# Kernel tuning notes

Hardware: AMD Instinct MI355X
Metric: run time of the kernel (lower is better)

The kernel has to match this reference:

```python
import jax, jax.numpy as jnp
import numpy as np

DIM = 1024
HEADS = 8
DIM_HEAD = 64
HIDDEN = HEADS * DIM_HEAD  # 512
SCALE = DIM_HEAD ** -0.5
BATCH = 16384
EPS = 1e-12  # F.normalize eps


def setup_inputs() -> dict:
    key = jax.random.key(0)
    k0, k1, k2 = jax.random.split(key, 3)
    x = jax.random.normal(k0, (BATCH, DIM), dtype=jnp.float32)
    w_qkv = jax.random.normal(k1, (3 * HIDDEN, DIM), dtype=jnp.float32) * 0.02
    w_out = jax.random.normal(k2, (DIM, HIDDEN), dtype=jnp.float32) * 0.02
    b_out = jnp.zeros((DIM,), dtype=jnp.float32)
    g = jnp.ones((1, DIM), dtype=jnp.float32)
    return {"x": x, "w_qkv": w_qkv, "w_out": w_out, "b_out": b_out, "g": g}


def reference(x, w_qkv, w_out, b_out, g):
    b = x.shape[0]
    # Conv1d(kernel=1, no bias) on n=1 sequence == matmul with (3*hidden, dim) weight
    qkv = x @ w_qkv.T  # (b, 3*hidden)
    q, k, v = jnp.split(qkv, 3, axis=1)  # each (b, hidden)
    # rearrange 'b (h c) n -> b h c n' with n=1 -> (b, h, c)
    q = q.reshape(b, HEADS, DIM_HEAD)
    k = k.reshape(b, HEADS, DIM_HEAD)
    v = v.reshape(b, HEADS, DIM_HEAD)
    # q.softmax(dim=-2) is over the c axis
    q = jax.nn.softmax(q, axis=-1) * SCALE
    # k.softmax(dim=-1) is over the n axis of size 1 -> all ones (kept faithful)
    k = jax.nn.softmax(k[..., None], axis=-1)[..., 0]
    # context = einsum('bhdn,bhen->bhde', k, v); out = einsum('bhde,bhdn->bhen', context, q)
    # with n=1 this collapses to out_e = (sum_d k_d q_d) * v_e; fused to avoid (b,h,d,e)
    s = jnp.einsum('bhd,bhd->bh', k, q)  # (b, h)
    out = s[..., None] * v  # (b, h, e)
    out = out.reshape(b, HIDDEN)  # 'b h c n -> b (h c) n', squeeze(-1)
    # Linear(hidden, dim)
    out = out @ w_out.T + b_out  # (b, dim)
    # RMSNorm_MLP: F.normalize(x, dim=1) * g * sqrt(dim)
    norm = jnp.linalg.norm(out, axis=1, keepdims=True)
    out = out / jnp.maximum(norm, EPS) * g * jnp.sqrt(jnp.float32(DIM))
    return out
```

## Files before the change

kernel.cpp:

```cpp
#include <hip/hip_runtime.h>
#include <hip/hip_bf16.h>


typedef __attribute__((ext_vector_type(8))) short bf16x8;
typedef __attribute__((ext_vector_type(4))) float f32x4;

struct alignas(16) bfvec8 { __hip_bfloat16 h[8]; };

__device__ __forceinline__ bfvec8 pack8(float4 a, float4 b) {
    bfvec8 o;
    o.h[0] = __float2bfloat16(a.x); o.h[1] = __float2bfloat16(a.y);
    o.h[2] = __float2bfloat16(a.z); o.h[3] = __float2bfloat16(a.w);
    o.h[4] = __float2bfloat16(b.x); o.h[5] = __float2bfloat16(b.y);
    o.h[6] = __float2bfloat16(b.z); o.h[7] = __float2bfloat16(b.w);
    return o;
}

__global__ __launch_bounds__(256)
void prep(const float* __restrict__ Wo, const float* __restrict__ Wv,
          __hip_bfloat16* __restrict__ Weff,
          const float* __restrict__ X, __hip_bfloat16* __restrict__ Xbf) {
    __shared__ __align__(16) __hip_bfloat16 As[64 * 32];
    __shared__ __align__(16) __hip_bfloat16 Bs[64 * 32];
    __shared__ __align__(16) float Bf[32 * 65];

    const int tid = threadIdx.x;

    if (blockIdx.x >= 256) {
        const size_t nv = (size_t)16384 * 1024 / 8;
        const size_t stride = (size_t)2048 * 256;
        for (size_t i = (size_t)(blockIdx.x - 256) * 256 + tid; i < nv; i += stride) {
            const float4 a = *(const float4*)(X + i * 8);
            const float4 b = *(const float4*)(X + i * 8 + 4);
            *(bfvec8*)(Xbf + i * 8) = pack8(a, b);
        }
        return;
    }

    const int lane = tid & 63;
    const int wave = tid >> 6;
    const int wm   = wave >> 1;
    const int wn   = wave & 1;
    const int quad = lane >> 4;
    const int tr   = lane & 15;
    const int m0   = (blockIdx.x >> 4) * 64;
    const int n0   = (blockIdx.x & 15) * 64;

    f32x4 acc[2][2];
#pragma unroll
    for (int i = 0; i < 2; ++i)
#pragma unroll
        for (int j = 0; j < 2; ++j)
            acc[i][j] = (f32x4){0.f, 0.f, 0.f, 0.f};

    for (int kt = 0; kt < 512; kt += 32) {
        {
            int r = tid >> 2, c = tid & 3;
            int s = (r >> 1) & 3;
            int kg = (c ^ s) << 3;
            const float* sp = Wo + (size_t)(m0 + r) * 512 + kt + kg;
            float4 a = *(const float4*)sp, b = *(const float4*)(sp + 4);
            *(bfvec8*)(As + r * 32 + (c << 3)) = pack8(a, b);
        }
        {
            int kr = tid >> 3, c8 = (tid & 7) << 3;
            const float* sp = Wv + (size_t)(kt + kr) * 1024 + n0 + c8;
            float4 a = *(const float4*)sp, b = *(const float4*)(sp + 4);
            *(float4*)(Bf + kr * 65 + c8)     = a;
            *(float4*)(Bf + kr * 65 + c8 + 4) = b;
        }
        __syncthreads();
        {
            int n = tid >> 2, cc = tid & 3, k8 = cc << 3;
            float4 a, b;
            a.x = Bf[(k8 + 0) * 65 + n]; a.y = Bf[(k8 + 1) * 65 + n];
            a.z = Bf[(k8 + 2) * 65 + n]; a.w = Bf[(k8 + 3) * 65 + n];
            b.x = Bf[(k8 + 4) * 65 + n]; b.y = Bf[(k8 + 5) * 65 + n];
            b.z = Bf[(k8 + 6) * 65 + n]; b.w = Bf[(k8 + 7) * 65 + n];
            int cs = cc ^ ((n >> 1) & 3);
            *(bfvec8*)(Bs + n * 32 + cs * 8) = pack8(a, b);
        }
        __syncthreads();

        bf16x8 af[2], bfr[2];
#pragma unroll
        for (int mi = 0; mi < 2; ++mi) {
            int r = wm * 32 + mi * 16 + tr;
            int c = quad ^ ((r >> 1) & 3);
            af[mi] = *(const bf16x8*)(As + r * 32 + c * 8);
        }
#pragma unroll
        for (int ni = 0; ni < 2; ++ni) {
            int r = wn * 32 + ni * 16 + tr;
            int c = quad ^ ((r >> 1) & 3);
            bfr[ni] = *(const bf16x8*)(Bs + r * 32 + c * 8);
        }
#pragma unroll
        for (int mi = 0; mi < 2; ++mi)
#pragma unroll
            for (int ni = 0; ni < 2; ++ni)
                acc[mi][ni] = __builtin_amdgcn_mfma_f32_16x16x32_bf16(
                    af[mi], bfr[ni], acc[mi][ni], 0, 0, 0);
        __syncthreads();
    }

#pragma unroll
    for (int mi = 0; mi < 2; ++mi)
#pragma unroll
        for (int ni = 0; ni < 2; ++ni) {
            const int col = n0 + wn * 32 + ni * 16 + tr;
#pragma unroll
            for (int r = 0; r < 4; ++r) {
                const int row = m0 + wm * 32 + mi * 16 + quad * 4 + r;
                Weff[(size_t)row * 1024 + col] =
                    __float2bfloat16(acc[mi][ni][r] * 0.125f);
            }
        }
}


#define GLL(gp, lp) __builtin_amdgcn_global_load_lds( \
    (const __attribute__((address_space(1))) void*)(gp), \
    (__attribute__((address_space(3))) void*)(lp), 16, 0, 0)

#define STAGE_A(BUF, H, U) do { \
    GLL(Xbf + Ab0 + (size_t)(H) * 131072 + (size_t)(U) * 64, \
        sm + (BUF) * 32768 + (H) * 8192 + ldsA);             \
    GLL(Xbf + Ab1 + (size_t)(H) * 131072 + (size_t)(U) * 64, \
        sm + (BUF) * 32768 + (H) * 8192 + 4096 + ldsA);      \
} while (0)

#define STAGE_B(BUF, H, U) do { \
    GLL(Bt + Bb0 + (size_t)(H) * 131072 + (size_t)(U) * 64,  \
        sm + (BUF) * 32768 + 16384 + (H) * 8192 + ldsA);     \
    GLL(Bt + Bb1 + (size_t)(H) * 131072 + (size_t)(U) * 64,  \
        sm + (BUF) * 32768 + 16384 + (H) * 8192 + 4096 + ldsA); \
} while (0)

__global__ __launch_bounds__(512, 2)
void main_gemm(const __hip_bfloat16* __restrict__ Xbf,
               const __hip_bfloat16* __restrict__ Bt,
               const float* __restrict__ bias,
               __hip_bfloat16* __restrict__ Y) {
    __shared__ __align__(16) __hip_bfloat16 sm[2 * 32768];

    const int tid  = threadIdx.x;
    const int lane = tid & 63;
    const int wc   = tid >> 6;
    const int quad = lane >> 4;
    const int tr   = lane & 15;
    const int rlow = tr & 7;

    const int xcd  = blockIdx.x & 7;
    const int orig = xcd * 32 + (blockIdx.x >> 3);
    const int m0   = (orig >> 2) * 256;
    const int n0   = (orig & 3) * 256;

    const int r0 = tid >> 3,            c0 = tid & 7;
    const int r1 = (tid + 512) >> 3,    c1 = tid & 7;
    const size_t Ab0 = (size_t)(m0 + r0) * 1024 + ((c0 ^ (r0 & 7)) << 3);
    const size_t Ab1 = (size_t)(m0 + r1) * 1024 + ((c1 ^ (r1 & 7)) << 3);
    const size_t Bb0 = (size_t)(n0 + r0) * 1024 + ((c0 ^ (r0 & 7)) << 3);
    const size_t Bb1 = (size_t)(n0 + r1) * 1024 + ((c1 ^ (r1 & 7)) << 3);
    const int ldsA = tid * 8;

    int ac[2];
#pragma unroll
    for (int ko = 0; ko < 2; ++ko) ac[ko] = ((ko * 4 + quad) ^ rlow) * 8;
    const int rdA = tr * 64;
    const int rdB = wc * 2048 + tr * 64;

    f32x4 acc[16][2];
#pragma unroll
    for (int f = 0; f < 16; ++f)
#pragma unroll
        for (int ni = 0; ni < 2; ++ni)
            acc[f][ni] = (f32x4){0.f, 0.f, 0.f, 0.f};

    STAGE_B(0, 0, 0); STAGE_B(0, 1, 0); STAGE_A(0, 0, 0); STAGE_A(0, 1, 0);
    STAGE_B(1, 0, 1); STAGE_B(1, 1, 1); STAGE_A(1, 0, 1);
    asm volatile("s_waitcnt vmcnt(6)" ::: "memory");
    __builtin_amdgcn_s_barrier();

    bf16x8 bfr[2][2];

    for (int it = 0; it < 8; ++it) {
#pragma unroll
        for (int rb = 0; rb < 2; ++rb) {
            const int u = it * 2 + rb;
#pragma unroll
            for (int p = 0; p < 4; ++p) {
                bf16x8 af[4][2];
#pragma unroll
                for (int mi = 0; mi < 4; ++mi)
#pragma unroll
                    for (int ko = 0; ko < 2; ++ko)
                        af[mi][ko] = *(const bf16x8*)(
                            sm + rb * 32768 + p * 4096 + mi * 1024 + rdA + ac[ko]);
                if (p == 0) {
#pragma unroll
                    for (int ni = 0; ni < 2; ++ni)
#pragma unroll
                        for (int ko = 0; ko < 2; ++ko)
                            bfr[ni][ko] = *(const bf16x8*)(
                                sm + rb * 32768 + 16384 + rdB + ni * 1024 + ac[ko]);
                }

                if (p == 0)      { if (u + 1 < 16) STAGE_A(rb ^ 1, 1, u + 1); }
                else if (p == 1) { if (u + 2 < 16) STAGE_B(rb, 0, u + 2); }
                else if (p == 2) { if (u + 2 < 16) STAGE_B(rb, 1, u + 2); }
                else             { if (u + 2 < 16) STAGE_A(rb, 0, u + 2); }

                if (p == 0) asm volatile("s_waitcnt lgkmcnt(8)" ::: "memory");
                __builtin_amdgcn_s_barrier();
                asm volatile("s_waitcnt lgkmcnt(0)" ::: "memory");
                __builtin_amdgcn_sched_barrier(0);

                __builtin_amdgcn_s_setprio(1);
#pragma unroll
                for (int mi = 0; mi < 4; ++mi)
#pragma unroll
                    for (int ni = 0; ni < 2; ++ni)
#pragma unroll
                        for (int ko = 0; ko < 2; ++ko)
                            acc[p * 4 + mi][ni] = __builtin_amdgcn_mfma_f32_16x16x32_bf16(
                                af[mi][ko], bfr[ni][ko], acc[p * 4 + mi][ni], 0, 0, 0);
                __builtin_amdgcn_s_setprio(0);

                if (p == 3) {
                    if (u <= 13)      asm volatile("s_waitcnt vmcnt(6)" ::: "memory");
                    else if (u == 14) asm volatile("s_waitcnt vmcnt(0)" ::: "memory");
                    if (u < 15) __builtin_amdgcn_s_barrier();
                } else {
                    __builtin_amdgcn_s_barrier();
                }
            }
        }
    }

    float bv[2]; int col[2];
#pragma unroll
    for (int ni = 0; ni < 2; ++ni) {
        col[ni] = n0 + wc * 32 + ni * 16 + tr;
        bv[ni]  = bias[col[ni]];
    }
#pragma unroll
    for (int f = 0; f < 16; ++f)
#pragma unroll
        for (int ni = 0; ni < 2; ++ni)
#pragma unroll
            for (int rr = 0; rr < 4; ++rr) {
                const int row = m0 + f * 16 + quad * 4 + rr;
                Y[(size_t)row * 1024 + col[ni]] =
                    __float2bfloat16(acc[f][ni][rr] + bv[ni]);
            }
}

__global__ __launch_bounds__(256)
void rmsnorm2(const __hip_bfloat16* __restrict__ y, const float* __restrict__ g,
              float* __restrict__ out) {
    const int wave = threadIdx.x >> 6;
    const int sub  = wave >> 1;
    const int t    = threadIdx.x & 127;
    const int row  = blockIdx.x * 2 + sub;
    const size_t base = (size_t)row * 1024 + t * 8;

    union { uint4 u; ushort s[8]; } U;
    U.u = *(const uint4*)(y + base);
    float v[8];
#pragma unroll
    for (int j = 0; j < 8; ++j)
        v[j] = __bfloat162float(*(const __hip_bfloat16*)&U.s[j]);

    float ss = 0.f;
#pragma unroll
    for (int j = 0; j < 8; ++j) ss += v[j] * v[j];
#pragma unroll
    for (int off = 32; off > 0; off >>= 1)
        ss += __shfl_down(ss, off, 64);

    __shared__ float wsum[4];
    if ((threadIdx.x & 63) == 0) wsum[wave] = ss;
    __syncthreads();
    const float total = wsum[sub * 2] + wsum[sub * 2 + 1];
    const float sc = 32.0f / fmaxf(sqrtf(total), 1e-12f);

    const float4 g0 = *(const float4*)(g + t * 8);
    const float4 g1 = *(const float4*)(g + t * 8 + 4);
    float4 o0, o1;
    o0.x = v[0] * sc * g0.x; o0.y = v[1] * sc * g0.y;
    o0.z = v[2] * sc * g0.z; o0.w = v[3] * sc * g0.w;
    o1.x = v[4] * sc * g1.x; o1.y = v[5] * sc * g1.y;
    o1.z = v[6] * sc * g1.z; o1.w = v[7] * sc * g1.w;
    *(float4*)(out + base)     = o0;
    *(float4*)(out + base + 4) = o1;
}

extern "C" void kernel_launch(void* const* d_in, const int* in_sizes, int n_in,
                              void* d_out, int out_size, void* d_ws, size_t ws_size,
                              hipStream_t stream) {
    const float* x     = (const float*)d_in[0];
    const float* w_qkv = (const float*)d_in[1];
    const float* w_out = (const float*)d_in[2];
    const float* b_out = (const float*)d_in[3];
    const float* g     = (const float*)d_in[4];

    const int B = 16384, D = 1024, H = 512;
    const float* wv = w_qkv + (size_t)2 * H * D;

    char* ws = (char*)d_ws;
    size_t off = 0;
    __hip_bfloat16* weff_bf = (__hip_bfloat16*)(ws + off); off += (size_t)D * D * 2;
    __hip_bfloat16* y_bf    = (__hip_bfloat16*)(ws + off); off += (size_t)B * D * 2;
    __hip_bfloat16* x_bf    = (__hip_bfloat16*)(ws + off); off += (size_t)B * D * 2;

    prep<<<256 + 2048, 256, 0, stream>>>(w_out, wv, weff_bf, x, x_bf);
    main_gemm<<<256, 512, 0, stream>>>(x_bf, weff_bf, b_out, y_bf);
    rmsnorm2<<<B / 2, 256, 0, stream>>>(y_bf, g, (float*)d_out);
}
```

Measured before the change: 178.4 us.

## Fuse RMSNorm into GEMM epilogue via cooperative grid sync

```diff
diff --git a/kernel.cpp b/kernel.cpp
--- a/kernel.cpp
+++ b/kernel.cpp
@@ -1,5 +1,8 @@
 #include <hip/hip_runtime.h>
 #include <hip/hip_bf16.h>
+#include <hip/hip_cooperative_groups.h>
+
+namespace cg = cooperative_groups;
 
 
 typedef __attribute__((ext_vector_type(8))) short bf16x8;
@@ -138,11 +141,15 @@
 } while (0)
 
 __global__ __launch_bounds__(512, 2)
-void main_gemm(const __hip_bfloat16* __restrict__ Xbf,
-               const __hip_bfloat16* __restrict__ Bt,
-               const float* __restrict__ bias,
-               __hip_bfloat16* __restrict__ Y) {
+void main_fused(const __hip_bfloat16* __restrict__ Xbf,
+                const __hip_bfloat16* __restrict__ Bt,
+                const float* __restrict__ bias,
+                const float* __restrict__ g,
+                float* __restrict__ partial,
+                float* __restrict__ out) {
     __shared__ __align__(16) __hip_bfloat16 sm[2 * 32768];
+    __shared__ float wpart[8][256];
+    __shared__ float scs[256];
 
     const int tid  = threadIdx.x;
     const int lane = tid & 63;
@@ -155,6 +162,7 @@
     const int orig = xcd * 32 + (blockIdx.x >> 3);
     const int m0   = (orig >> 2) * 256;
     const int n0   = (orig & 3) * 256;
+    const int ntl  = orig & 3;
 
     const int r0 = tid >> 3,            c0 = tid & 7;
     const int r1 = (tid + 512) >> 3,    c1 = tid & 7;
@@ -247,53 +255,49 @@
 #pragma unroll
     for (int f = 0; f < 16; ++f)
 #pragma unroll
-        for (int ni = 0; ni < 2; ++ni)
-#pragma unroll
-            for (int rr = 0; rr < 4; ++rr) {
-                const int row = m0 + f * 16 + quad * 4 + rr;
-                Y[(size_t)row * 1024 + col[ni]] =
-                    __float2bfloat16(acc[f][ni][rr] + bv[ni]);
+        for (int rr = 0; rr < 4; ++rr) {
+            float v = 0.f;
+#pragma unroll
+            for (int ni = 0; ni < 2; ++ni) {
+                acc[f][ni][rr] += bv[ni];
+                v += acc[f][ni][rr] * acc[f][ni][rr];
             }
-}
-
-__global__ __launch_bounds__(256)
-void rmsnorm2(const __hip_bfloat16* __restrict__ y, const float* __restrict__ g,
-              float* __restrict__ out) {
-    const int wave = threadIdx.x >> 6;
-    const int sub  = wave >> 1;
-    const int t    = threadIdx.x & 127;
-    const int row  = blockIdx.x * 2 + sub;
-    const size_t base = (size_t)row * 1024 + t * 8;
-
-    union { uint4 u; ushort s[8]; } U;
-    U.u = *(const uint4*)(y + base);
-    float v[8];
-#pragma unroll
-    for (int j = 0; j < 8; ++j)
-        v[j] = __bfloat162float(*(const __hip_bfloat16*)&U.s[j]);
-
-    float ss = 0.f;
-#pragma unroll
-    for (int j = 0; j < 8; ++j) ss += v[j] * v[j];
-#pragma unroll
-    for (int off = 32; off > 0; off >>= 1)
-        ss += __shfl_down(ss, off, 64);
-
-    __shared__ float wsum[4];
-    if ((threadIdx.x & 63) == 0) wsum[wave] = ss;
+#pragma unroll
+            for (int msk = 1; msk < 16; msk <<= 1)
+                v += __shfl_xor(v, msk, 64);
+            if (tr == 0) wpart[wc][f * 16 + quad * 4 + rr] = v;
+        }
     __syncthreads();
-    const float total = wsum[sub * 2] + wsum[sub * 2 + 1];
-    const float sc = 32.0f / fmaxf(sqrtf(total), 1e-12f);
-
-    const float4 g0 = *(const float4*)(g + t * 8);
-    const float4 g1 = *(const float4*)(g + t * 8 + 4);
-    float4 o0, o1;
-    o0.x = v[0] * sc * g0.x; o0.y = v[1] * sc * g0.y;
-    o0.z = v[2] * sc * g0.z; o0.w = v[3] * sc * g0.w;
-    o1.x = v[4] * sc * g1.x; o1.y = v[5] * sc * g1.y;
-    o1.z = v[6] * sc * g1.z; o1.w = v[7] * sc * g1.w;
-    *(float4*)(out + base)     = o0;
-    *(float4*)(out + base + 4) = o1;
+    if (tid < 256) {
+        float s = 0.f;
+#pragma unroll
+        for (int w = 0; w < 8; ++w) s += wpart[w][tid];
+        partial[(size_t)(m0 + tid) * 4 + ntl] = s;
+    }
+
+    cg::this_grid().sync();
+
+    if (tid < 256) {
+        const float* pr = partial + (size_t)(m0 + tid) * 4;
+        const float s = pr[0] + pr[1] + pr[2] + pr[3];
+        scs[tid] = 32.0f / fmaxf(sqrtf(s), 1e-12f);
+    }
+    __syncthreads();
+
+    float gv[2];
+#pragma unroll
+    for (int ni = 0; ni < 2; ++ni) gv[ni] = g[col[ni]];
+#pragma unroll
+    for (int f = 0; f < 16; ++f)
+#pragma unroll
+        for (int rr = 0; rr < 4; ++rr) {
+            const int rowin = f * 16 + quad * 4 + rr;
+            const float sc = scs[rowin];
+#pragma unroll
+            for (int ni = 0; ni < 2; ++ni)
+                out[(size_t)(m0 + rowin) * 1024 + col[ni]] =
+                    acc[f][ni][rr] * sc * gv[ni];
+        }
 }
 
 extern "C" void kernel_launch(void* const* d_in, const int* in_sizes, int n_in,
@@ -311,10 +315,20 @@
     char* ws = (char*)d_ws;
     size_t off = 0;
     __hip_bfloat16* weff_bf = (__hip_bfloat16*)(ws + off); off += (size_t)D * D * 2;
-    __hip_bfloat16* y_bf    = (__hip_bfloat16*)(ws + off); off += (size_t)B * D * 2;
     __hip_bfloat16* x_bf    = (__hip_bfloat16*)(ws + off); off += (size_t)B * D * 2;
+    float*          part    = (float*)(ws + off);          off += (size_t)B * 4 * 4;
 
     prep<<<256 + 2048, 256, 0, stream>>>(w_out, wv, weff_bf, x, x_bf);
-    main_gemm<<<256, 512, 0, stream>>>(x_bf, weff_bf, b_out, y_bf);
-    rmsnorm2<<<B / 2, 256, 0, stream>>>(y_bf, g, (float*)d_out);
+
+    {
+        const __hip_bfloat16* a0 = x_bf;
+        const __hip_bfloat16* a1 = weff_bf;
+        const float* a2 = b_out;
+        const float* a3 = g;
+        float* a4 = part;
+        float* a5 = (float*)d_out;
+        void* args[] = {&a0, &a1, &a2, &a3, &a4, &a5};
+        hipLaunchCooperativeKernel((void*)main_fused, dim3(256), dim3(512),
+                                   args, 0, stream);
+    }
 }
```

Result: slower. 223.0 us (+25.0%).

## Fuse fp32-to-bf16 conversion of X into the main GEMM's A-tile loading

Applied to the files above, without the earlier changes.

```diff
diff --git a/kernel.cpp b/kernel.cpp
--- a/kernel.cpp
+++ b/kernel.cpp
@@ -17,26 +17,13 @@
 }
 
 __global__ __launch_bounds__(256)
-void prep(const float* __restrict__ Wo, const float* __restrict__ Wv,
-          __hip_bfloat16* __restrict__ Weff,
-          const float* __restrict__ X, __hip_bfloat16* __restrict__ Xbf) {
+void weff_only(const float* __restrict__ Wo, const float* __restrict__ Wv,
+               __hip_bfloat16* __restrict__ Weff) {
     __shared__ __align__(16) __hip_bfloat16 As[64 * 32];
     __shared__ __align__(16) __hip_bfloat16 Bs[64 * 32];
     __shared__ __align__(16) float Bf[32 * 65];
 
-    const int tid = threadIdx.x;
-
-    if (blockIdx.x >= 256) {
-        const size_t nv = (size_t)16384 * 1024 / 8;
-        const size_t stride = (size_t)2048 * 256;
-        for (size_t i = (size_t)(blockIdx.x - 256) * 256 + tid; i < nv; i += stride) {
-            const float4 a = *(const float4*)(X + i * 8);
-            const float4 b = *(const float4*)(X + i * 8 + 4);
-            *(bfvec8*)(Xbf + i * 8) = pack8(a, b);
-        }
-        return;
-    }
-
+    const int tid  = threadIdx.x;
     const int lane = tid & 63;
     const int wave = tid >> 6;
     const int wm   = wave >> 1;
@@ -123,22 +110,31 @@
     (const __attribute__((address_space(1))) void*)(gp), \
     (__attribute__((address_space(3))) void*)(lp), 16, 0, 0)
 
-#define STAGE_A(BUF, H, U) do { \
-    GLL(Xbf + Ab0 + (size_t)(H) * 131072 + (size_t)(U) * 64, \
-        sm + (BUF) * 32768 + (H) * 8192 + ldsA);             \
-    GLL(Xbf + Ab1 + (size_t)(H) * 131072 + (size_t)(U) * 64, \
-        sm + (BUF) * 32768 + (H) * 8192 + 4096 + ldsA);      \
-} while (0)
-
 #define STAGE_B(BUF, H, U) do { \
     GLL(Bt + Bb0 + (size_t)(H) * 131072 + (size_t)(U) * 64,  \
-        sm + (BUF) * 32768 + 16384 + (H) * 8192 + ldsA);     \
+        sm + (BUF) * 32768 + 16384 + (H) * 8192 + tid * 8);  \
     GLL(Bt + Bb1 + (size_t)(H) * 131072 + (size_t)(U) * 64,  \
-        sm + (BUF) * 32768 + 16384 + (H) * 8192 + 4096 + ldsA); \
+        sm + (BUF) * 32768 + 16384 + (H) * 8192 + 4096 + tid * 8); \
 } while (0)
 
+#define LOAD_A(U) do { \
+    _Pragma("unroll") \
+    for (int j = 0; j < 4; ++j) { \
+        const float* s_ = Xrow + (size_t)(U) * 64 + aoff[j]; \
+        pa[2*j]   = *(const float4*)s_; \
+        pa[2*j+1] = *(const float4*)(s_ + 4); \
+    } \
+} while (0)
+
+#define WRITE_A(BUF) do { \
+    _Pragma("unroll") \
+    for (int j = 0; j < 4; ++j) \
+        *(bfvec8*)(sm + (BUF) * 32768 + tid * 32 + j * 8) = \
+            pack8(pa[2*j], pa[2*j+1]); \
+} while (0)
+
 __global__ __launch_bounds__(512, 2)
-void main_gemm(const __hip_bfloat16* __restrict__ Xbf,
+void main_gemm(const float* __restrict__ X,
                const __hip_bfloat16* __restrict__ Bt,
                const float* __restrict__ bias,
                __hip_bfloat16* __restrict__ Y) {
@@ -156,13 +152,17 @@
     const int m0   = (orig >> 2) * 256;
     const int n0   = (orig & 3) * 256;
 
-    const int r0 = tid >> 3,            c0 = tid & 7;
-    const int r1 = (tid + 512) >> 3,    c1 = tid & 7;
-    const size_t Ab0 = (size_t)(m0 + r0) * 1024 + ((c0 ^ (r0 & 7)) << 3);
-    const size_t Ab1 = (size_t)(m0 + r1) * 1024 + ((c1 ^ (r1 & 7)) << 3);
+    const int r0 = tid >> 3,         c0 = tid & 7;
+    const int r1 = (tid + 512) >> 3, c1 = tid & 7;
     const size_t Bb0 = (size_t)(n0 + r0) * 1024 + ((c0 ^ (r0 & 7)) << 3);
     const size_t Bb1 = (size_t)(n0 + r1) * 1024 + ((c1 ^ (r1 & 7)) << 3);
-    const int ldsA = tid * 8;
+
+    const int  Ra   = tid >> 1;
+    const float* Xrow = X + (size_t)(m0 + Ra) * 1024;
+    int aoff[4];
+#pragma unroll
+    for (int j = 0; j < 4; ++j)
+        aoff[j] = ((((tid & 1) * 4 + j) ^ (Ra & 7)) << 3);
 
     int ac[2];
 #pragma unroll
@@ -177,9 +177,19 @@
         for (int ni = 0; ni < 2; ++ni)
             acc[f][ni] = (f32x4){0.f, 0.f, 0.f, 0.f};
 
-    STAGE_B(0, 0, 0); STAGE_B(0, 1, 0); STAGE_A(0, 0, 0); STAGE_A(0, 1, 0);
-    STAGE_B(1, 0, 1); STAGE_B(1, 1, 1); STAGE_A(1, 0, 1);
-    asm volatile("s_waitcnt vmcnt(6)" ::: "memory");
+    float4 pa[8];
+
+    LOAD_A(0);
+    __builtin_amdgcn_sched_barrier(0);
+    STAGE_B(0, 0, 0); STAGE_B(0, 1, 0);
+    STAGE_B(1, 0, 1); STAGE_B(1, 1, 1);
+    __builtin_amdgcn_sched_barrier(0);
+    asm volatile("s_waitcnt vmcnt(8)" ::: "memory");
+    WRITE_A(0);
+    __builtin_amdgcn_sched_barrier(0);
+    LOAD_A(1);
+    __builtin_amdgcn_sched_barrier(0);
+    asm volatile("s_waitcnt vmcnt(8) lgkmcnt(0)" ::: "memory");
     __builtin_amdgcn_s_barrier();
 
     bf16x8 bfr[2][2];
@@ -206,10 +216,19 @@
                                 sm + rb * 32768 + 16384 + rdB + ni * 1024 + ac[ko]);
                 }
 
-                if (p == 0)      { if (u + 1 < 16) STAGE_A(rb ^ 1, 1, u + 1); }
-                else if (p == 1) { if (u + 2 < 16) STAGE_B(rb, 0, u + 2); }
-                else if (p == 2) { if (u + 2 < 16) STAGE_B(rb, 1, u + 2); }
-                else             { if (u + 2 < 16) STAGE_A(rb, 0, u + 2); }
+                if (p == 1)      { if (u <= 13) STAGE_B(rb, 0, u + 2); }
+                else if (p == 2) { if (u <= 13) STAGE_B(rb, 1, u + 2); }
+                else if (p == 3) {
+                    if (u <= 14) {
+                        if (u <= 13) asm volatile("s_waitcnt vmcnt(4)" ::: "memory");
+                        else         asm volatile("s_waitcnt vmcnt(0)" ::: "memory");
+                        __builtin_amdgcn_sched_barrier(0);
+                        WRITE_A(rb ^ 1);
+                        __builtin_amdgcn_sched_barrier(0);
+                        if (u <= 13) LOAD_A(u + 2);
+                        __builtin_amdgcn_sched_barrier(0);
+                    }
+                }
 
                 if (p == 0) asm volatile("s_waitcnt lgkmcnt(8)" ::: "memory");
                 __builtin_amdgcn_s_barrier();
@@ -228,8 +247,6 @@
                 __builtin_amdgcn_s_setprio(0);
 
                 if (p == 3) {
-                    if (u <= 13)      asm volatile("s_waitcnt vmcnt(6)" ::: "memory");
-                    else if (u == 14) asm volatile("s_waitcnt vmcnt(0)" ::: "memory");
                     if (u < 15) __builtin_amdgcn_s_barrier();
                 } else {
                     __builtin_amdgcn_s_barrier();
@@ -312,9 +329,8 @@
     size_t off = 0;
     __hip_bfloat16* weff_bf = (__hip_bfloat16*)(ws + off); off += (size_t)D * D * 2;
     __hip_bfloat16* y_bf    = (__hip_bfloat16*)(ws + off); off += (size_t)B * D * 2;
-    __hip_bfloat16* x_bf    = (__hip_bfloat16*)(ws + off); off += (size_t)B * D * 2;
-
-    prep<<<256 + 2048, 256, 0, stream>>>(w_out, wv, weff_bf, x, x_bf);
-    main_gemm<<<256, 512, 0, stream>>>(x_bf, weff_bf, b_out, y_bf);
+
+    weff_only<<<256, 256, 0, stream>>>(w_out, wv, weff_bf);
+    main_gemm<<<256, 512, 0, stream>>>(x, weff_bf, b_out, y_bf);
     rmsnorm2<<<B / 2, 256, 0, stream>>>(y_bf, g, (float*)d_out);
 }
```

After: 209.6 us. 17.5% more time.
